# Kernel tuning notes

Measured on AMD Instinct MI355X. Metric: run time of the kernel, lower is better.

## Reference

```python
import jax, jax.numpy as jnp
import numpy as np

GAMMA = 2          # relu(cos_sim)**gamma, from init gamma=2
EPS = 1e-8         # torch CosineSimilarity eps (norm clamp)
B, C, H, WID = 4, 256, 64, 64


def setup_inputs() -> dict:
    key = jax.random.key(0)
    kx, kw = jax.random.split(key)
    x = jax.random.normal(kx, (B, C, H, WID), dtype=jnp.float32)
    # 1x1 conv (nlayers=1): weight [C_out, C_in], bias [C_out]
    W = jax.random.normal(kw, (C, C), dtype=jnp.float32) * 0.02
    b = jnp.zeros((C,), dtype=jnp.float32)
    return {"x": x, "W": W, "b": b}


def reference(x, W, b):
    # x: [B,C,H,W]. Flatten pixels: p/q index (h*W+w).
    Bs, Cs, Hs, Ws = x.shape
    xf = x.reshape(Bs, Cs, Hs * Ws)                      # [B,C,P]
    norm = jnp.sqrt(jnp.sum(xf * xf, axis=1, keepdims=True))
    xn = xf / jnp.maximum(norm, EPS)                     # channel-normalized
    # full pairwise cosine similarity over pixels, relu, power gamma
    s = jax.nn.relu(jnp.einsum('bcp,bcq->bpq', xn, xn)) ** GAMMA  # [B,P,Q]
    # transform: 1x1 conv = per-pixel linear map over channels
    gx = jnp.einsum('oc,bcp->bop', W, xf) + b[None, :, None]      # [B,C,P]
    # y[b,c,p] = sum_q s[b,p,q] * gx[b,c,q]  (== 'bijhw,bchw->bcij')
    y = jnp.einsum('bpq,bcq->bcp', s, gx)
    return y.reshape(Bs, Cs, Hs, Ws)
```

## Files before the change

kernel.cpp:

```cpp
#include <hip/hip_runtime.h>

#define BN 4
#define CN 256
#define PN 4096
#define QT 32
#define TSTR 264

typedef __attribute__((ext_vector_type(8))) short short8;
typedef __attribute__((ext_vector_type(8))) unsigned short ushort8;
typedef __attribute__((ext_vector_type(4))) float f32x4;
typedef __attribute__((ext_vector_type(4))) unsigned int u32x4;
typedef unsigned int u32;

__device__ __forceinline__ unsigned short f2bf(float f) {
  u32 u = __builtin_bit_cast(u32, f);
  return (unsigned short)((u + 0x7fffu + ((u >> 16) & 1u)) >> 16);
}

__device__ __forceinline__ void async_copy16(const void* g, void* l) {
  __builtin_amdgcn_global_load_lds((const __attribute__((address_space(1))) u32*)g,
                                   (__attribute__((address_space(3))) u32*)l, 16, 0, 0);
}


__global__ __launch_bounds__(256) void k_nx(const float* __restrict__ x,
                                            float* __restrict__ mnorm,
                                            unsigned short* __restrict__ xnK) {
  __shared__ unsigned short tl[64 * TSTR];
  __shared__ float red[4][64];
  const int b = blockIdx.y, qb = blockIdx.x, p0 = qb * 64;
  const int tid = threadIdx.x;
  const int tp = tid & 63, cg = tid >> 6;
  const float* xp = x + ((size_t)b * CN + cg * 64) * PN + p0 + tp;
  float v[64];
  float ss = 0.f;
#pragma unroll
  for (int i = 0; i < 64; ++i) {
    v[i] = xp[(size_t)i * PN];
    ss += v[i] * v[i];
  }
  red[cg][tp] = ss;
  __syncthreads();
  float nrm = sqrtf(red[0][tp] + red[1][tp] + red[2][tp] + red[3][tp]);
  float mn = fmaxf(nrm, 1e-8f);
  float rn = 1.f / mn;
  if (cg == 0) mnorm[b * PN + p0 + tp] = mn;
  unsigned int* tl32 = (unsigned int*)tl;
#pragma unroll
  for (int j = 0; j < 32; ++j) {
    unsigned int w = (unsigned int)f2bf(v[2 * j] * rn) |
                     ((unsigned int)f2bf(v[2 * j + 1] * rn) << 16);
    tl32[tp * (TSTR / 2) + cg * 32 + j] = w;
  }
  __syncthreads();
  char* dstb = (char*)xnK + (size_t)b * (PN * CN * 2) + (size_t)qb * 32768;
#pragma unroll
  for (int m = 0; m < 8; ++m) {
    int idx = m * 256 + tid;
    int F = idx >> 6, ln = idx & 63;
    int pl = (F >> 3) * 16 + (ln & 15);
    int ch = (F & 7) * 32 + (ln >> 4) * 8;
    ushort8 o = *(const ushort8*)(tl + pl * TSTR + ch);
    *(ushort8*)(dstb + (size_t)idx * 16) = o;
  }
}

__global__ void k_gx(const float* __restrict__ Wm, const float* __restrict__ bias,
                     const unsigned short* __restrict__ xnK, const float* __restrict__ mnorm,
                     unsigned short* __restrict__ gxF) {
  const int b = blockIdx.z;
  const int m0 = blockIdx.y * 64;
  const int qb = blockIdx.x, q0 = qb * 64;
  const int tid = threadIdx.x;
  const int wave = tid >> 6, lane = tid & 63;
  const int lr = lane & 15, g = lane >> 4;

  short8 af[8];
  {
    const float* wr = Wm + (size_t)(m0 + wave * 16 + lr) * CN;
#pragma unroll
    for (int k = 0; k < 8; ++k) {
      const float* ap = wr + k * 32 + g * 8;
      short8 a;
#pragma unroll
      for (int j = 0; j < 8; ++j) a[j] = (short)f2bf(ap[j]);
      af[k] = a;
    }
  }
  f32x4 acc[4];
#pragma unroll
  for (int n = 0; n < 4; ++n) acc[n] = (f32x4){0.f, 0.f, 0.f, 0.f};

  const char* xb = (const char*)xnK + (size_t)b * (PN * CN * 2) + (size_t)qb * 32768;
#pragma unroll
  for (int n = 0; n < 4; ++n)
#pragma unroll
    for (int k = 0; k < 8; ++k) {
      short8 bf = *(const short8*)(xb + ((n * 8 + k) << 10) + ((g * 16 + lr) << 4));
      acc[n] = __builtin_amdgcn_mfma_f32_16x16x32_bf16(af[k], bf, acc[n], 0, 0, 0);
    }
  char* vbb = (char*)gxF + (size_t)b * (PN * CN * 2) + (size_t)qb * 32768;
#pragma unroll
  for (int n = 0; n < 4; ++n) {
    int q = q0 + n * 16 + lr;
    float mn = mnorm[b * PN + q];
    int kk = n >> 1;
    int q32 = (n & 1) * 16 + lr;
    int gp = (q32 >> 2) & 3;
    int j = ((q32 >> 4) & 1) * 4 + (q32 & 3);
#pragma unroll
    for (int i = 0; i < 4; ++i) {
      int c = m0 + wave * 16 + g * 4 + i;
      float v = acc[n][i] * mn + bias[c];
      *(unsigned short*)(vbb + ((kk * 16 + (c >> 4)) << 10) + (gp << 8) + ((c & 15) << 4) + (j << 1)) = f2bf(v);
    }
  }
}

extern __shared__ char smem[];

__global__ __launch_bounds__(256, 2) void k_attn(const unsigned short* __restrict__ xnK,
                                                 const unsigned short* __restrict__ gxF,
                                                 float* __restrict__ d0, float* __restrict__ d1,
                                                 float* __restrict__ d2, float* __restrict__ d3,
                                                 int lq, int ntiles) {
  const int fid = blockIdx.x;
  const int b = fid & 3;
  const int qs = (fid >> 2) & ((1 << lq) - 1);
  const int pblk = fid >> (2 + lq);
  const int tid = threadIdx.x;
  const int wave = tid >> 6, lane = tid & 63, lr = lane & 15, g = lane >> 4;
  const int p0 = pblk * 128 + wave * 32;
  float* dst = (qs == 0) ? d0 : (qs == 1) ? d1 : (qs == 2) ? d2 : d3;

  const char* xb = (const char*)xnK + (size_t)b * (PN * CN * 2);
  const char* vg = (const char*)gxF + (size_t)b * (PN * CN * 2);
  const int qt0 = (qs * (PN >> lq)) >> 5;
  const char* kq = xb + (size_t)qt0 * 16384;
  const char* vq = vg + (size_t)qt0 * 16384;
  const int ldst = tid * 16;
  const int lane16 = lane * 16;

  auto issue_K = [&](int t) {
    char* kb = smem + (t & 1) * 32768;
    const char* s = kq + (size_t)t * 16384 + ldst;
#pragma unroll
    for (int j = 0; j < 4; ++j) async_copy16(s + j * 4096, kb + ldst + j * 4096);
  };
  auto issue_V = [&](int t) {
    char* vb = smem + (t & 1) * 32768 + 16384;
    const char* s = vq + (size_t)t * 16384 + ldst;
#pragma unroll
    for (int j = 0; j < 4; ++j) async_copy16(s + j * 4096, vb + ldst + j * 4096);
  };

  issue_K(0);
  issue_V(0);

  short8 qf[2][8];
  {
    const char* qpb = xb + (size_t)(pblk * 2 + (wave >> 1)) * 32768;
#pragma unroll
    for (int mt = 0; mt < 2; ++mt) {
      int ntp = (wave & 1) * 2 + mt;
#pragma unroll
      for (int k = 0; k < 8; ++k)
        qf[mt][k] = *(const short8*)(qpb + ((ntp * 8 + k) << 10) + ((g * 16 + lr) << 4));
    }
  }

  f32x4 yacc[2][16];
#pragma unroll
  for (int mt = 0; mt < 2; ++mt)
#pragma unroll
    for (int n = 0; n < 16; ++n) yacc[mt][n] = (f32x4){0.f, 0.f, 0.f, 0.f};

  for (int t = 0; t < ntiles; ++t) {
    const char* kb = smem + (t & 1) * 32768;
    const char* vb = kb + 16384;

    asm volatile("s_waitcnt vmcnt(4)" ::: "memory");
    __builtin_amdgcn_s_barrier();
    if (t + 1 < ntiles) { issue_K(t + 1); issue_V(t + 1); }

    f32x4 sacc[2][2];
#pragma unroll
    for (int n0 = 0; n0 < 2; ++n0)
#pragma unroll
      for (int mt = 0; mt < 2; ++mt) sacc[n0][mt] = (f32x4){0.f, 0.f, 0.f, 0.f};
    __builtin_amdgcn_s_setprio(1);
#pragma unroll
    for (int k = 0; k < 8; ++k) {
      short8 kf0 = *(const short8*)(kb + k * 1024 + lane16);
      short8 kf1 = *(const short8*)(kb + (8 + k) * 1024 + lane16);
      sacc[0][0] = __builtin_amdgcn_mfma_f32_16x16x32_bf16(kf0, qf[0][k], sacc[0][0], 0, 0, 0);
      sacc[0][1] = __builtin_amdgcn_mfma_f32_16x16x32_bf16(kf0, qf[1][k], sacc[0][1], 0, 0, 0);
      sacc[1][0] = __builtin_amdgcn_mfma_f32_16x16x32_bf16(kf1, qf[0][k], sacc[1][0], 0, 0, 0);
      sacc[1][1] = __builtin_amdgcn_mfma_f32_16x16x32_bf16(kf1, qf[1][k], sacc[1][1], 0, 0, 0);
    }
    __builtin_amdgcn_s_setprio(0);

    u32 pa[2][4];
#pragma unroll
    for (int mt = 0; mt < 2; ++mt)
#pragma unroll
      for (int n0 = 0; n0 < 2; ++n0)
#pragma unroll
        for (int h = 0; h < 2; ++h) {
          float a0 = fmaxf(sacc[n0][mt][2 * h], 0.f);
          a0 *= a0;
          float a1 = fmaxf(sacc[n0][mt][2 * h + 1], 0.f);
          a1 *= a1;
          u32 w;
          asm("v_cvt_pk_bf16_f32 %0, %1, %2" : "=v"(w) : "v"(a0), "v"(a1));
          pa[mt][n0 * 2 + h] = w;
        }

    if (t + 1 < ntiles) {
      asm volatile("s_waitcnt vmcnt(8)" ::: "memory");
    } else {
      asm volatile("s_waitcnt vmcnt(0)" ::: "memory");
    }
    __builtin_amdgcn_s_barrier();

    u32x4 w0 = {pa[0][0], pa[0][1], pa[0][2], pa[0][3]};
    u32x4 w1 = {pa[1][0], pa[1][1], pa[1][2], pa[1][3]};
    short8 a0 = __builtin_bit_cast(short8, w0);
    short8 a1 = __builtin_bit_cast(short8, w1);
    __builtin_amdgcn_s_setprio(1);
#pragma unroll
    for (int n2 = 0; n2 < 16; ++n2) {
      short8 vf = *(const short8*)(vb + n2 * 1024 + lane16);
      yacc[0][n2] = __builtin_amdgcn_mfma_f32_16x16x32_bf16(a0, vf, yacc[0][n2], 0, 0, 0);
      yacc[1][n2] = __builtin_amdgcn_mfma_f32_16x16x32_bf16(a1, vf, yacc[1][n2], 0, 0, 0);
    }
    __builtin_amdgcn_s_setprio(0);
  }
  __builtin_amdgcn_s_barrier();

  float* yl = (float*)(smem + wave * 16384);
  const int row8 = lane >> 3, p4 = (lane & 7) << 2;
#pragma unroll
  for (int cc = 0; cc < 4; ++cc) {
#pragma unroll
    for (int nn = 0; nn < 4; ++nn)
#pragma unroll
      for (int mt = 0; mt < 2; ++mt)
#pragma unroll
        for (int i = 0; i < 4; ++i)
          yl[(nn * 16 + lr) * 33 + mt * 16 + g * 4 + i] = yacc[mt][cc * 4 + nn][i];
#pragma unroll
    for (int r2 = 0; r2 < 8; ++r2) {
      int c = r2 * 8 + row8;
      float4 v = *(const float4*)(yl + c * 33 + p4);
      *(float4*)(dst + ((size_t)b * CN + cc * 64 + c) * PN + p0 + p4) = v;
    }
  }
}

__global__ void k_add(float* __restrict__ o, const float* __restrict__ a,
                      const float* __restrict__ bb, const float* __restrict__ c,
                      int np, int n4) {
  int i = blockIdx.x * blockDim.x + threadIdx.x;
  int stride = gridDim.x * blockDim.x;
  float4* o4 = (float4*)o;
  const float4* a4 = (const float4*)a;
  const float4* b4 = (const float4*)bb;
  const float4* c4 = (const float4*)c;
  for (; i < n4; i += stride) {
    float4 r = o4[i];
    float4 va = a4[i];
    r.x += va.x; r.y += va.y; r.z += va.z; r.w += va.w;
    if (np > 1) {
      float4 vb = b4[i];
      r.x += vb.x; r.y += vb.y; r.z += vb.z; r.w += vb.w;
      float4 vc = c4[i];
      r.x += vc.x; r.y += vc.y; r.z += vc.z; r.w += vc.w;
    }
    o4[i] = r;
  }
}

extern "C" void kernel_launch(void* const* d_in, const int* in_sizes, int n_in,
                              void* d_out, int out_size, void* d_ws, size_t ws_size,
                              hipStream_t stream) {
  const float* x = (const float*)d_in[0];
  const float* Wm = (const float*)d_in[1];
  const float* bias = (const float*)d_in[2];
  float* out = (float*)d_out;

  char* ws = (char*)d_ws;
  unsigned short* xnK = (unsigned short*)ws;
  unsigned short* gxF = (unsigned short*)(ws + (size_t)8388608);
  float* mnorm = (float*)(ws + (size_t)16777216);
  float* yp0 = (float*)(ws + (size_t)16842752);
  float* yp1 = yp0 + 4194304;
  float* yp2 = yp1 + 4194304;
  const size_t need4 = 16842752ULL + 3ULL * 16777216ULL;

  hipFuncSetAttribute(reinterpret_cast<const void*>(k_attn),
                      hipFuncAttributeMaxDynamicSharedMemorySize, 65536);

  k_nx<<<dim3(PN / 64, BN), 256, 0, stream>>>(x, mnorm, xnK);
  k_gx<<<dim3(PN / 64, CN / 64, BN), 256, 0, stream>>>(Wm, bias, xnK, mnorm, gxF);
  if (ws_size >= need4) {
    k_attn<<<dim3(512), 256, 65536, stream>>>(xnK, gxF, out, yp0, yp1, yp2, 2, (PN / 4) / QT);
    k_add<<<dim3(1024), 256, 0, stream>>>(out, yp0, yp1, yp2, 3, BN * CN * PN / 4);
  } else {
    k_attn<<<dim3(256), 256, 65536, stream>>>(xnK, gxF, out, yp0, yp0, yp0, 1, (PN / 2) / QT);
    k_add<<<dim3(1024), 256, 0, stream>>>(out, yp0, yp0, yp0, 1, BN * CN * PN / 4);
  }
}
```

Baseline: 104.9 us.

## Software-pipeline attention with triple buffering, 512-thread blocks and fp16 partials

Restructures the attention kernel so that the S=QK tile for step t is computed in the same MFMA loop as the PV accumulation for step t-1. K/V tiles are triple-buffered in LDS (96KB) and loaded by 512-thread blocks that cover 256 pixels each. The split-Q partial outputs (other than the first) are stored as fp16 instead of fp32, which halves the partial write and read traffic in the final add kernel. In exchange it adds fp16 rounding error on the partials, raises LDS use per block, and halves the grid size.

```diff
diff --git a/kernel.cpp b/kernel.cpp
--- a/kernel.cpp
+++ b/kernel.cpp
@@ -1,4 +1,5 @@
 #include <hip/hip_runtime.h>
+#include <hip/hip_fp16.h>
 
 #define BN 4
 #define CN 256
@@ -8,6 +9,7 @@
 
 typedef __attribute__((ext_vector_type(8))) short short8;
 typedef __attribute__((ext_vector_type(8))) unsigned short ushort8;
+typedef __attribute__((ext_vector_type(4))) unsigned short us4;
 typedef __attribute__((ext_vector_type(4))) float f32x4;
 typedef __attribute__((ext_vector_type(4))) unsigned int u32x4;
 typedef unsigned int u32;
@@ -119,10 +121,11 @@
 
 extern __shared__ char smem[];
 
-__global__ __launch_bounds__(256, 2) void k_attn(const unsigned short* __restrict__ xnK,
+__global__ __launch_bounds__(512, 2) void k_attn(const unsigned short* __restrict__ xnK,
                                                  const unsigned short* __restrict__ gxF,
-                                                 float* __restrict__ d0, float* __restrict__ d1,
-                                                 float* __restrict__ d2, float* __restrict__ d3,
+                                                 float* __restrict__ out,
+                                                 __half* __restrict__ p1, __half* __restrict__ p2,
+                                                 __half* __restrict__ p3,
                                                  int lq, int ntiles) {
   const int fid = blockIdx.x;
   const int b = fid & 3;
@@ -130,36 +133,32 @@
   const int pblk = fid >> (2 + lq);
   const int tid = threadIdx.x;
   const int wave = tid >> 6, lane = tid & 63, lr = lane & 15, g = lane >> 4;
-  const int p0 = pblk * 128 + wave * 32;
-  float* dst = (qs == 0) ? d0 : (qs == 1) ? d1 : (qs == 2) ? d2 : d3;
+  const int p0 = pblk * 256 + wave * 32;
+  __half* dsth = (qs == 1) ? p1 : (qs == 2) ? p2 : p3;
 
   const char* xb = (const char*)xnK + (size_t)b * (PN * CN * 2);
-  const char* vg = (const char*)gxF + (size_t)b * (PN * CN * 2);
+  const char* vgb = (const char*)gxF + (size_t)b * (PN * CN * 2);
   const int qt0 = (qs * (PN >> lq)) >> 5;
   const char* kq = xb + (size_t)qt0 * 16384;
-  const char* vq = vg + (size_t)qt0 * 16384;
+  const char* vq = vgb + (size_t)qt0 * 16384;
   const int ldst = tid * 16;
   const int lane16 = lane * 16;
 
-  auto issue_K = [&](int t) {
-    char* kb = smem + (t & 1) * 32768;
-    const char* s = kq + (size_t)t * 16384 + ldst;
-#pragma unroll
-    for (int j = 0; j < 4; ++j) async_copy16(s + j * 4096, kb + ldst + j * 4096);
+  auto issue = [&](int t) {
+    char* buf = smem + (t % 3) * 32768;
+    const char* ks = kq + (size_t)t * 16384 + ldst;
+    const char* vs = vq + (size_t)t * 16384 + ldst;
+    async_copy16(ks, buf + ldst);
+    async_copy16(ks + 8192, buf + ldst + 8192);
+    async_copy16(vs, buf + 16384 + ldst);
+    async_copy16(vs + 8192, buf + 16384 + ldst + 8192);
   };
-  auto issue_V = [&](int t) {
-    char* vb = smem + (t & 1) * 32768 + 16384;
-    const char* s = vq + (size_t)t * 16384 + ldst;
-#pragma unroll
-    for (int j = 0; j < 4; ++j) async_copy16(s + j * 4096, vb + ldst + j * 4096);
-  };
-
-  issue_K(0);
-  issue_V(0);
+
+  issue(0);
 
   short8 qf[2][8];
   {
-    const char* qpb = xb + (size_t)(pblk * 2 + (wave >> 1)) * 32768;
+    const char* qpb = xb + (size_t)(pblk * 4 + (wave >> 1)) * 32768;
 #pragma unroll
     for (int mt = 0; mt < 2; ++mt) {
       int ntp = (wave & 1) * 2 + mt;
@@ -175,14 +174,13 @@
 #pragma unroll
     for (int n = 0; n < 16; ++n) yacc[mt][n] = (f32x4){0.f, 0.f, 0.f, 0.f};
 
-  for (int t = 0; t < ntiles; ++t) {
-    const char* kb = smem + (t & 1) * 32768;
-    const char* vb = kb + 16384;
-
-    asm volatile("s_waitcnt vmcnt(4)" ::: "memory");
+  u32 pa[2][4];
+
+  {
+    const char* kb = smem;
+    asm volatile("s_waitcnt vmcnt(2)" ::: "memory");
     __builtin_amdgcn_s_barrier();
-    if (t + 1 < ntiles) { issue_K(t + 1); issue_V(t + 1); }
-
+    issue(1);
     f32x4 sacc[2][2];
 #pragma unroll
     for (int n0 = 0; n0 < 2; ++n0)
@@ -199,30 +197,73 @@
       sacc[1][1] = __builtin_amdgcn_mfma_f32_16x16x32_bf16(kf1, qf[1][k], sacc[1][1], 0, 0, 0);
     }
     __builtin_amdgcn_s_setprio(0);
-
-    u32 pa[2][4];
 #pragma unroll
     for (int mt = 0; mt < 2; ++mt)
 #pragma unroll
       for (int n0 = 0; n0 < 2; ++n0)
 #pragma unroll
         for (int h = 0; h < 2; ++h) {
-          float a0 = fmaxf(sacc[n0][mt][2 * h], 0.f);
-          a0 *= a0;
-          float a1 = fmaxf(sacc[n0][mt][2 * h + 1], 0.f);
-          a1 *= a1;
+          float a0 = fmaxf(sacc[n0][mt][2 * h], 0.f); a0 *= a0;
+          float a1 = fmaxf(sacc[n0][mt][2 * h + 1], 0.f); a1 *= a1;
           u32 w;
           asm("v_cvt_pk_bf16_f32 %0, %1, %2" : "=v"(w) : "v"(a0), "v"(a1));
           pa[mt][n0 * 2 + h] = w;
         }
-
-    if (t + 1 < ntiles) {
-      asm volatile("s_waitcnt vmcnt(8)" ::: "memory");
-    } else {
-      asm volatile("s_waitcnt vmcnt(0)" ::: "memory");
-    }
+  }
+
+  for (int t = 1; t < ntiles; ++t) {
+    const char* kb = smem + (t % 3) * 32768;
+    const char* vbp = smem + ((t + 2) % 3) * 32768 + 16384;
+    asm volatile("s_waitcnt vmcnt(2)" ::: "memory");
     __builtin_amdgcn_s_barrier();
-
+    if (t + 1 < ntiles) issue(t + 1);
+
+    u32x4 w0 = {pa[0][0], pa[0][1], pa[0][2], pa[0][3]};
+    u32x4 w1 = {pa[1][0], pa[1][1], pa[1][2], pa[1][3]};
+    short8 a0 = __builtin_bit_cast(short8, w0);
+    short8 a1 = __builtin_bit_cast(short8, w1);
+
+    f32x4 sacc[2][2];
+#pragma unroll
+    for (int n0 = 0; n0 < 2; ++n0)
+#pragma unroll
+      for (int mt = 0; mt < 2; ++mt) sacc[n0][mt] = (f32x4){0.f, 0.f, 0.f, 0.f};
+    __builtin_amdgcn_s_setprio(1);
+#pragma unroll
+    for (int k = 0; k < 8; ++k) {
+      short8 kf0 = *(const short8*)(kb + k * 1024 + lane16);
+      short8 kf1 = *(const short8*)(kb + (8 + k) * 1024 + lane16);
+      sacc[0][0] = __builtin_amdgcn_mfma_f32_16x16x32_bf16(kf0, qf[0][k], sacc[0][0], 0, 0, 0);
+      sacc[0][1] = __builtin_amdgcn_mfma_f32_16x16x32_bf16(kf0, qf[1][k], sacc[0][1], 0, 0, 0);
+      sacc[1][0] = __builtin_amdgcn_mfma_f32_16x16x32_bf16(kf1, qf[0][k], sacc[1][0], 0, 0, 0);
+      sacc[1][1] = __builtin_amdgcn_mfma_f32_16x16x32_bf16(kf1, qf[1][k], sacc[1][1], 0, 0, 0);
+      short8 vf0 = *(const short8*)(vbp + (2 * k) * 1024 + lane16);
+      short8 vf1 = *(const short8*)(vbp + (2 * k + 1) * 1024 + lane16);
+      yacc[0][2 * k] = __builtin_amdgcn_mfma_f32_16x16x32_bf16(a0, vf0, yacc[0][2 * k], 0, 0, 0);
+      yacc[1][2 * k] = __builtin_amdgcn_mfma_f32_16x16x32_bf16(a1, vf0, yacc[1][2 * k], 0, 0, 0);
+      yacc[0][2 * k + 1] = __builtin_amdgcn_mfma_f32_16x16x32_bf16(a0, vf1, yacc[0][2 * k + 1], 0, 0, 0);
+      yacc[1][2 * k + 1] = __builtin_amdgcn_mfma_f32_16x16x32_bf16(a1, vf1, yacc[1][2 * k + 1], 0, 0, 0);
+    }
+    __builtin_amdgcn_s_setprio(0);
+
+#pragma unroll
+    for (int mt = 0; mt < 2; ++mt)
+#pragma unroll
+      for (int n0 = 0; n0 < 2; ++n0)
+#pragma unroll
+        for (int h = 0; h < 2; ++h) {
+          float a2 = fmaxf(sacc[n0][mt][2 * h], 0.f); a2 *= a2;
+          float a3 = fmaxf(sacc[n0][mt][2 * h + 1], 0.f); a3 *= a3;
+          u32 w;
+          asm("v_cvt_pk_bf16_f32 %0, %1, %2" : "=v"(w) : "v"(a2), "v"(a3));
+          pa[mt][n0 * 2 + h] = w;
+        }
+  }
+
+  asm volatile("s_waitcnt vmcnt(0)" ::: "memory");
+  __builtin_amdgcn_s_barrier();
+  {
+    const char* vbl = smem + ((ntiles - 1) % 3) * 32768 + 16384;
     u32x4 w0 = {pa[0][0], pa[0][1], pa[0][2], pa[0][3]};
     u32x4 w1 = {pa[1][0], pa[1][1], pa[1][2], pa[1][3]};
     short8 a0 = __builtin_bit_cast(short8, w0);
@@ -230,7 +271,7 @@
     __builtin_amdgcn_s_setprio(1);
 #pragma unroll
     for (int n2 = 0; n2 < 16; ++n2) {
-      short8 vf = *(const short8*)(vb + n2 * 1024 + lane16);
+      short8 vf = *(const short8*)(vbl + n2 * 1024 + lane16);
       yacc[0][n2] = __builtin_amdgcn_mfma_f32_16x16x32_bf16(a0, vf, yacc[0][n2], 0, 0, 0);
       yacc[1][n2] = __builtin_amdgcn_mfma_f32_16x16x32_bf16(a1, vf, yacc[1][n2], 0, 0, 0);
     }
@@ -238,7 +279,7 @@
   }
   __builtin_amdgcn_s_barrier();
 
-  float* yl = (float*)(smem + wave * 16384);
+  float* yl = (float*)(smem + wave * 12288);
   const int row8 = lane >> 3, p4 = (lane & 7) << 2;
 #pragma unroll
   for (int cc = 0; cc < 4; ++cc) {
@@ -253,29 +294,45 @@
     for (int r2 = 0; r2 < 8; ++r2) {
       int c = r2 * 8 + row8;
       float4 v = *(const float4*)(yl + c * 33 + p4);
-      *(float4*)(dst + ((size_t)b * CN + cc * 64 + c) * PN + p0 + p4) = v;
-    }
-  }
-}
-
-__global__ void k_add(float* __restrict__ o, const float* __restrict__ a,
-                      const float* __restrict__ bb, const float* __restrict__ c,
+      size_t off = ((size_t)b * CN + cc * 64 + c) * PN + p0 + p4;
+      if (qs == 0) {
+        *(float4*)(out + off) = v;
+      } else {
+        us4 h;
+        h[0] = __builtin_bit_cast(unsigned short, __float2half(v.x));
+        h[1] = __builtin_bit_cast(unsigned short, __float2half(v.y));
+        h[2] = __builtin_bit_cast(unsigned short, __float2half(v.z));
+        h[3] = __builtin_bit_cast(unsigned short, __float2half(v.w));
+        *(us4*)(dsth + off) = h;
+      }
+    }
+  }
+}
+
+__global__ void k_add(float* __restrict__ o, const unsigned int* __restrict__ a,
+                      const unsigned int* __restrict__ bb, const unsigned int* __restrict__ c,
                       int np, int n4) {
   int i = blockIdx.x * blockDim.x + threadIdx.x;
   int stride = gridDim.x * blockDim.x;
   float4* o4 = (float4*)o;
-  const float4* a4 = (const float4*)a;
-  const float4* b4 = (const float4*)bb;
-  const float4* c4 = (const float4*)c;
+  const uint2* a2 = (const uint2*)a;
+  const uint2* b2 = (const uint2*)bb;
+  const uint2* c2 = (const uint2*)c;
   for (; i < n4; i += stride) {
     float4 r = o4[i];
-    float4 va = a4[i];
-    r.x += va.x; r.y += va.y; r.z += va.z; r.w += va.w;
+    uint2 ua = a2[i];
+    float2 f0 = __half22float2(__builtin_bit_cast(__half2, ua.x));
+    float2 f1 = __half22float2(__builtin_bit_cast(__half2, ua.y));
+    r.x += f0.x; r.y += f0.y; r.z += f1.x; r.w += f1.y;
     if (np > 1) {
-      float4 vb = b4[i];
-      r.x += vb.x; r.y += vb.y; r.z += vb.z; r.w += vb.w;
-      float4 vc = c4[i];
-      r.x += vc.x; r.y += vc.y; r.z += vc.z; r.w += vc.w;
+      uint2 ub = b2[i];
+      f0 = __half22float2(__builtin_bit_cast(__half2, ub.x));
+      f1 = __half22float2(__builtin_bit_cast(__half2, ub.y));
+      r.x += f0.x; r.y += f0.y; r.z += f1.x; r.w += f1.y;
+      uint2 uc = c2[i];
+      f0 = __half22float2(__builtin_bit_cast(__half2, uc.x));
+      f1 = __half22float2(__builtin_bit_cast(__half2, uc.y));
+      r.x += f0.x; r.y += f0.y; r.z += f1.x; r.w += f1.y;
     }
     o4[i] = r;
   }
@@ -293,21 +350,23 @@
   unsigned short* xnK = (unsigned short*)ws;
   unsigned short* gxF = (unsigned short*)(ws + (size_t)8388608);
   float* mnorm = (float*)(ws + (size_t)16777216);
-  float* yp0 = (float*)(ws + (size_t)16842752);
-  float* yp1 = yp0 + 4194304;
-  float* yp2 = yp1 + 4194304;
-  const size_t need4 = 16842752ULL + 3ULL * 16777216ULL;
+  __half* p1 = (__half*)(ws + (size_t)16842752);
+  __half* p2 = p1 + 4194304;
+  __half* p3 = p2 + 4194304;
+  const size_t need4 = 16842752ULL + 3ULL * 8388608ULL;
 
   hipFuncSetAttribute(reinterpret_cast<const void*>(k_attn),
-                      hipFuncAttributeMaxDynamicSharedMemorySize, 65536);
+                      hipFuncAttributeMaxDynamicSharedMemorySize, 98304);
 
   k_nx<<<dim3(PN / 64, BN), 256, 0, stream>>>(x, mnorm, xnK);
   k_gx<<<dim3(PN / 64, CN / 64, BN), 256, 0, stream>>>(Wm, bias, xnK, mnorm, gxF);
   if (ws_size >= need4) {
-    k_attn<<<dim3(512), 256, 65536, stream>>>(xnK, gxF, out, yp0, yp1, yp2, 2, (PN / 4) / QT);
-    k_add<<<dim3(1024), 256, 0, stream>>>(out, yp0, yp1, yp2, 3, BN * CN * PN / 4);
+    k_attn<<<dim3(256), 512, 98304, stream>>>(xnK, gxF, out, p1, p2, p3, 2, (PN / 4) / QT);
+    k_add<<<dim3(1024), 256, 0, stream>>>(out, (const unsigned int*)p1, (const unsigned int*)p2,
+                                          (const unsigned int*)p3, 3, BN * CN * PN / 4);
   } else {
-    k_attn<<<dim3(256), 256, 65536, stream>>>(xnK, gxF, out, yp0, yp0, yp0, 1, (PN / 2) / QT);
-    k_add<<<dim3(1024), 256, 0, stream>>>(out, yp0, yp0, yp0, 1, BN * CN * PN / 4);
-  }
-}
+    k_attn<<<dim3(128), 512, 98304, stream>>>(xnK, gxF, out, p1, p1, p1, 1, (PN / 2) / QT);
+    k_add<<<dim3(1024), 256, 0, stream>>>(out, (const unsigned int*)p1, (const unsigned int*)p1,
+                                          (const unsigned int*)p1, 1, BN * CN * PN / 4);
+  }
+}
```

New measurement: 104.3 us. About the same (-0.6%).
